# Kernel tuning notes

Measured on AMD Instinct MI355X. Metric: run time of the kernel, lower is better.

## Reference

```python
import jax, jax.numpy as jnp
import numpy as np

MAX_N_LATENT = 8


def setup_inputs() -> dict:
    key = jax.random.key(0)
    k1, k2, k3 = jax.random.split(key, 3)
    B, S, D = 8, 4096, 1024
    latent_states = jax.random.normal(k1, (B, S, D), dtype=jnp.float32)
    binary_mask = jax.random.randint(k2, (B, S, 1), 0, 2, dtype=jnp.int32)
    W = jax.random.normal(k3, (D, D), dtype=jnp.float32) * (1.0 / np.sqrt(D))
    b = jnp.zeros((D,), dtype=jnp.float32)
    return {"latent_states": latent_states, "binary_mask": binary_mask, "W": W, "b": b}


def reference(latent_states, binary_mask, W, b):
    # latent_states: [B, S, D], binary_mask: [B, S, 1] in {0,1}
    m = binary_mask[..., 0]                       # [B, S] int
    # position i belongs to segment = #boundaries strictly before i (exclusive cumsum);
    # a position with mask==1 closes its own segment, next position starts a new one.
    seg = jnp.cumsum(m, axis=1) - m               # [B, S] exclusive cumsum
    # segments beyond MAX_N_LATENT are truncated -> route to dummy slot index 8
    segc = jnp.minimum(seg, MAX_N_LATENT)         # [B, S] in [0, 8]
    onehot = (segc[..., None] == jnp.arange(MAX_N_LATENT + 1)).astype(latent_states.dtype)  # [B, S, 9]
    sums = jnp.einsum('bsp,bsd->bpd', onehot, latent_states)   # [B, 9, D]
    counts = jnp.sum(onehot, axis=1)                            # [B, 9]
    mean = sums / jnp.maximum(counts, 1)[..., None]             # empty slots stay 0 (padding)
    patches = mean[:, :MAX_N_LATENT]                            # [B, 8, D]
    return patches @ W.T + b                                    # [B, 8, out_dim]
```

## Files before the change

kernel.cpp:

```cpp
#include <hip/hip_runtime.h>
#include <hip/hip_bf16.h>

#define SEQ 4096
#define DIM 1024

typedef __attribute__((ext_vector_type(8))) short short8;
typedef __attribute__((ext_vector_type(4))) float f32x4;
typedef __attribute__((ext_vector_type(4))) unsigned short us4;

__device__ __forceinline__ us4 cvt4(float a, float b, float c, float d) {
    union { us4 u; __hip_bfloat162 h[2]; } r;
    r.h[0] = __float22bfloat162_rn(make_float2(a, b));
    r.h[1] = __float22bfloat162_rn(make_float2(c, d));
    return r.u;
}

__global__ __launch_bounds__(512) void k_one(
    const float* __restrict__ latent,
    const int*   __restrict__ mask,
    const float* __restrict__ Wm,
    const float* __restrict__ bias,
    float*       __restrict__ out)
{
    __shared__ unsigned short sB[32 * 1024];
    __shared__ unsigned short sA[16 * 1024];
    __shared__ f32x4 sred[2][4][64];
    __shared__ int s_pos[8][8];

    const int blk  = blockIdx.x;
    const int b    = blk >> 5;
    const int ct   = blk & 31;
    const int tid  = threadIdx.x;
    const int lane = tid & 63;
    const int wid  = tid >> 6;

    const float4* wbase = (const float4*)(Wm + (size_t)(ct * 32) * DIM);
    float4 wv[16];
    #pragma unroll
    for (int i = 0; i < 16; ++i) wv[i] = wbase[i * 512 + tid];

    {
        if (lane < 8) s_pos[wid][lane] = SEQ;
        int carry = 0;
        for (int ch = 0; ch < SEQ / 256 && carry < 8; ++ch) {
            const int4 m = *(const int4*)(mask + (size_t)b * SEQ + ch * 256 + lane * 4);
            const int cnt = m.x + m.y + m.z + m.w;
            int v = cnt;
            #pragma unroll
            for (int off = 1; off < 64; off <<= 1) {
                int o = __shfl_up(v, off, 64);
                if (lane >= off) v += o;
            }
            const int excl = carry + v - cnt;
            if (excl < 8 && cnt > 0) {
                int vals[4] = {m.x, m.y, m.z, m.w};
                int rank = excl;
                #pragma unroll
                for (int i = 0; i < 4; ++i) {
                    if (vals[i]) {
                        if (rank < 8) s_pos[wid][rank] = ch * 256 + lane * 4 + i;
                        ++rank;
                    }
                }
            }
            carry += __shfl(v, 63, 64);
        }
    }

    #pragma unroll
    for (int i = 0; i < 16; ++i) {
        const int f  = i * 512 + tid;
        const int c  = f >> 8;
        const int k4 = f & 255;
        const int ks = k4 >> 3;
        const int lk = (k4 >> 1) & 3;
        const int j  = (k4 & 1) * 4;
        const int cg = c >> 4, l15 = c & 15;
        const int su = (lk * 16 + l15) ^ (ks & 7);
        *(us4*)&sB[cg * 16384 + ks * 512 + su * 8 + j] =
            cvt4(wv[i].x, wv[i].y, wv[i].z, wv[i].w);
    }

    for (int z = tid; z < 1024; z += 512) {
        const int ks  = z >> 5, idx = z & 31;
        const int su  = (idx & 7) + 8 + (idx >> 3) * 16;
        *(short8*)&sA[ks * 512 + su * 8] = (short8){0,0,0,0,0,0,0,0};
    }

    {
        const int p = wid;
        const int start = (p == 0) ? 0 : s_pos[wid][p - 1] + 1;
        const int endi  = min(s_pos[wid][p], SEQ - 1);
        const float4* lb = (const float4*)(latent + (size_t)b * SEQ * DIM);
        float4 A0 = {0,0,0,0}, A1 = {0,0,0,0}, A2 = {0,0,0,0}, A3 = {0,0,0,0};
        for (int r0 = start; r0 <= endi; r0 += 4) {
            float4 v[4][4];
            #pragma unroll
            for (int rr = 0; rr < 4; ++rr) {
                const int r = min(r0 + rr, endi);
                const float4* rp = lb + (size_t)r * (DIM / 4);
                v[rr][0] = rp[lane];       v[rr][1] = rp[64 + lane];
                v[rr][2] = rp[128 + lane]; v[rr][3] = rp[192 + lane];
            }
            #pragma unroll
            for (int rr = 0; rr < 4; ++rr) {
                if (r0 + rr > endi) break;
                A0.x += v[rr][0].x; A0.y += v[rr][0].y; A0.z += v[rr][0].z; A0.w += v[rr][0].w;
                A1.x += v[rr][1].x; A1.y += v[rr][1].y; A1.z += v[rr][1].z; A1.w += v[rr][1].w;
                A2.x += v[rr][2].x; A2.y += v[rr][2].y; A2.z += v[rr][2].z; A2.w += v[rr][2].w;
                A3.x += v[rr][3].x; A3.y += v[rr][3].y; A3.z += v[rr][3].z; A3.w += v[rr][3].w;
            }
        }
        const float inv = (endi >= start) ? 1.0f / (float)(endi - start + 1) : 0.0f;
        #pragma unroll
        for (int q = 0; q < 4; ++q) {
            const float4 aq = (q == 0) ? A0 : (q == 1) ? A1 : (q == 2) ? A2 : A3;
            const int t  = q * 64 + lane;
            const int ks = t >> 3;
            const int lk = (t >> 1) & 3;
            const int j  = (t & 1) * 4;
            const int su = (lk * 16 + p) ^ (ks & 7);
            *(us4*)&sA[ks * 512 + su * 8 + j] =
                cvt4(aq.x * inv, aq.y * inv, aq.z * inv, aq.w * inv);
        }
    }
    __syncthreads();

    const int cg = wid & 1;
    const int kh = wid >> 1;
    f32x4 acc = {0.f, 0.f, 0.f, 0.f};
    #pragma unroll
    for (int s = 0; s < 8; ++s) {
        const int ks = kh * 8 + s;
        const int sl = (lane ^ (ks & 7)) * 8;
        short8 a  = *(const short8*)&sA[ks * 512 + sl];
        short8 bb = *(const short8*)&sB[cg * 16384 + ks * 512 + sl];
        acc = __builtin_amdgcn_mfma_f32_16x16x32_bf16(a, bb, acc, 0, 0, 0);
    }

    if (kh != 0) sred[cg][kh][lane] = acc;
    __syncthreads();
    if (kh == 0) {
        f32x4 r1 = sred[cg][1][lane];
        f32x4 r2 = sred[cg][2][lane];
        f32x4 r3 = sred[cg][3][lane];
        acc = ((acc + r1) + r2) + r3;
        if (lane < 32) {
            const int l15 = lane & 15;
            const int lk2 = lane >> 4;
            const int col = ct * 32 + cg * 16 + l15;
            const float bv = bias[col];
            #pragma unroll
            for (int j = 0; j < 4; ++j)
                out[(size_t)(b * 8 + lk2 * 4 + j) * DIM + col] = acc[j] + bv;
        }
    }
}

extern "C" void kernel_launch(void* const* d_in, const int* in_sizes, int n_in,
                              void* d_out, int out_size, void* d_ws, size_t ws_size,
                              hipStream_t stream) {
    const float* latent = (const float*)d_in[0];
    const int*   mask   = (const int*)d_in[1];
    const float* Wm     = (const float*)d_in[2];
    const float* bias   = (const float*)d_in[3];
    float* out = (float*)d_out;

    k_one<<<256, 512, 0, stream>>>(latent, mask, Wm, bias, out);
}
```

Measured before the change: 10.54 us.

## Tile two batches per block with 16-column W tiles to fill MFMA rows

```diff
diff --git a/kernel.cpp b/kernel.cpp
--- a/kernel.cpp
+++ b/kernel.cpp
@@ -22,25 +22,27 @@
     const float* __restrict__ bias,
     float*       __restrict__ out)
 {
-    __shared__ unsigned short sB[32 * 1024];
+    __shared__ unsigned short sB[16 * 1024];
     __shared__ unsigned short sA[16 * 1024];
-    __shared__ f32x4 sred[2][4][64];
-    __shared__ int s_pos[8][8];
+    __shared__ f32x4 sred[8][64];
+    __shared__ int s_pos[8][2][8];
 
     const int blk  = blockIdx.x;
-    const int b    = blk >> 5;
-    const int ct   = blk & 31;
+    const int ct   = blk & 63;
+    const int bp   = blk >> 6;
     const int tid  = threadIdx.x;
     const int lane = tid & 63;
     const int wid  = tid >> 6;
 
-    const float4* wbase = (const float4*)(Wm + (size_t)(ct * 32) * DIM);
-    float4 wv[16];
+    const float4* wbase = (const float4*)(Wm + (size_t)(ct * 16) * DIM);
+    float4 wv[8];
     #pragma unroll
-    for (int i = 0; i < 16; ++i) wv[i] = wbase[i * 512 + tid];
+    for (int i = 0; i < 8; ++i) wv[i] = wbase[i * 512 + tid];
 
-    {
-        if (lane < 8) s_pos[wid][lane] = SEQ;
+    #pragma unroll
+    for (int bb = 0; bb < 2; ++bb) {
+        const int b = bp * 2 + bb;
+        if (lane < 8) s_pos[wid][bb][lane] = SEQ;
         int carry = 0;
         for (int ch = 0; ch < SEQ / 256 && carry < 8; ++ch) {
             const int4 m = *(const int4*)(mask + (size_t)b * SEQ + ch * 256 + lane * 4);
@@ -58,7 +60,7 @@
                 #pragma unroll
                 for (int i = 0; i < 4; ++i) {
                     if (vals[i]) {
-                        if (rank < 8) s_pos[wid][rank] = ch * 256 + lane * 4 + i;
+                        if (rank < 8) s_pos[wid][bb][rank] = ch * 256 + lane * 4 + i;
                         ++rank;
                     }
                 }
@@ -68,29 +70,24 @@
     }
 
     #pragma unroll
-    for (int i = 0; i < 16; ++i) {
+    for (int i = 0; i < 8; ++i) {
         const int f  = i * 512 + tid;
         const int c  = f >> 8;
         const int k4 = f & 255;
         const int ks = k4 >> 3;
         const int lk = (k4 >> 1) & 3;
         const int j  = (k4 & 1) * 4;
-        const int cg = c >> 4, l15 = c & 15;
-        const int su = (lk * 16 + l15) ^ (ks & 7);
-        *(us4*)&sB[cg * 16384 + ks * 512 + su * 8 + j] =
+        const int su = (lk * 16 + c) ^ (ks & 7);
+        *(us4*)&sB[ks * 512 + su * 8 + j] =
             cvt4(wv[i].x, wv[i].y, wv[i].z, wv[i].w);
     }
 
-    for (int z = tid; z < 1024; z += 512) {
-        const int ks  = z >> 5, idx = z & 31;
-        const int su  = (idx & 7) + 8 + (idx >> 3) * 16;
-        *(short8*)&sA[ks * 512 + su * 8] = (short8){0,0,0,0,0,0,0,0};
-    }
-
-    {
+    #pragma unroll
+    for (int bb = 0; bb < 2; ++bb) {
+        const int b = bp * 2 + bb;
         const int p = wid;
-        const int start = (p == 0) ? 0 : s_pos[wid][p - 1] + 1;
-        const int endi  = min(s_pos[wid][p], SEQ - 1);
+        const int start = (p == 0) ? 0 : s_pos[wid][bb][p - 1] + 1;
+        const int endi  = min(s_pos[wid][bb][p], SEQ - 1);
         const float4* lb = (const float4*)(latent + (size_t)b * SEQ * DIM);
         float4 A0 = {0,0,0,0}, A1 = {0,0,0,0}, A2 = {0,0,0,0}, A3 = {0,0,0,0};
         for (int r0 = start; r0 <= endi; r0 += 4) {
@@ -112,6 +109,7 @@
             }
         }
         const float inv = (endi >= start) ? 1.0f / (float)(endi - start + 1) : 0.0f;
+        const int rloc = bb * 8 + p;
         #pragma unroll
         for (int q = 0; q < 4; ++q) {
             const float4 aq = (q == 0) ? A0 : (q == 1) ? A1 : (q == 2) ? A2 : A3;
@@ -119,40 +117,41 @@
             const int ks = t >> 3;
             const int lk = (t >> 1) & 3;
             const int j  = (t & 1) * 4;
-            const int su = (lk * 16 + p) ^ (ks & 7);
+            const int su = (lk * 16 + rloc) ^ (ks & 7);
             *(us4*)&sA[ks * 512 + su * 8 + j] =
                 cvt4(aq.x * inv, aq.y * inv, aq.z * inv, aq.w * inv);
         }
     }
     __syncthreads();
 
-    const int cg = wid & 1;
-    const int kh = wid >> 1;
     f32x4 acc = {0.f, 0.f, 0.f, 0.f};
     #pragma unroll
-    for (int s = 0; s < 8; ++s) {
-        const int ks = kh * 8 + s;
+    for (int s = 0; s < 4; ++s) {
+        const int ks = wid * 4 + s;
         const int sl = (lane ^ (ks & 7)) * 8;
         short8 a  = *(const short8*)&sA[ks * 512 + sl];
-        short8 bb = *(const short8*)&sB[cg * 16384 + ks * 512 + sl];
+        short8 bb = *(const short8*)&sB[ks * 512 + sl];
         acc = __builtin_amdgcn_mfma_f32_16x16x32_bf16(a, bb, acc, 0, 0, 0);
     }
 
-    if (kh != 0) sred[cg][kh][lane] = acc;
+    if (wid != 0) sred[wid][lane] = acc;
     __syncthreads();
-    if (kh == 0) {
-        f32x4 r1 = sred[cg][1][lane];
-        f32x4 r2 = sred[cg][2][lane];
-        f32x4 r3 = sred[cg][3][lane];
-        acc = ((acc + r1) + r2) + r3;
-        if (lane < 32) {
-            const int l15 = lane & 15;
-            const int lk2 = lane >> 4;
-            const int col = ct * 32 + cg * 16 + l15;
-            const float bv = bias[col];
-            #pragma unroll
-            for (int j = 0; j < 4; ++j)
-                out[(size_t)(b * 8 + lk2 * 4 + j) * DIM + col] = acc[j] + bv;
+    if (wid == 0) {
+        #pragma unroll
+        for (int r = 1; r < 8; ++r) {
+            f32x4 o = sred[r][lane];
+            acc = acc + o;
+        }
+        const int l15 = lane & 15;
+        const int lk  = lane >> 4;
+        const int col = ct * 16 + l15;
+        const float bv = bias[col];
+        #pragma unroll
+        for (int j = 0; j < 4; ++j) {
+            const int rloc = lk * 4 + j;
+            const int b    = bp * 2 + (rloc >> 3);
+            const int p    = rloc & 7;
+            out[(size_t)(b * 8 + p) * DIM + col] = acc[j] + bv;
         }
     }
 }
```

Result: no change. 10.50 us (-0.4%).
